# Kernel optimization log

Hardware: AMD Instinct MI355X
Metric: run time of the kernel (lower is better)

## Reference

```python
import jax, jax.numpy as jnp
import numpy as np

COORD_DIM = 4
HIDDEN = 256
N_HIDDEN_LAYERS = 4  # num_layers - 1 hidden->hidden layers after the first
MIN_OMEGA = 10.0
MAX_OMEGA = 100.0
MEDIAN_OMEGA = (MIN_OMEGA + MAX_OMEGA) / 2.0
N = 524288


def _uniform(key, shape, bound):
    return jax.random.uniform(key, shape, jnp.float32, -bound, bound)


def setup_inputs() -> dict:
    key = jax.random.key(0)
    ks = jax.random.split(key, 16)
    coords = jax.random.normal(ks[0], (N, COORD_DIM), jnp.float32)
    # omega predictor: Linear(4, 64) -> ReLU -> Linear(64, 1) -> Sigmoid
    ow1 = _uniform(ks[1], (COORD_DIM, HIDDEN // 4), 1.0 / np.sqrt(COORD_DIM))
    ob1 = _uniform(ks[2], (HIDDEN // 4,), 1.0 / np.sqrt(COORD_DIM))
    ow2 = _uniform(ks[3], (HIDDEN // 4, 1), 1.0 / np.sqrt(HIDDEN // 4))
    ob2 = _uniform(ks[4], (1,), 1.0 / np.sqrt(HIDDEN // 4))
    # SIREN first layer: uniform(-1/in_features, 1/in_features)
    w0 = _uniform(ks[5], (COORD_DIM, HIDDEN), 1.0 / COORD_DIM)
    b0 = _uniform(ks[6], (HIDDEN,), 1.0 / np.sqrt(COORD_DIM))
    # SIREN hidden layers: uniform(-sqrt(6/in)/omega0, ...), stacked [4, 256, 256]
    hb = np.sqrt(6.0 / HIDDEN) / MEDIAN_OMEGA
    wh = _uniform(ks[7], (N_HIDDEN_LAYERS, HIDDEN, HIDDEN), hb)
    bh = _uniform(ks[8], (N_HIDDEN_LAYERS, HIDDEN), 1.0 / np.sqrt(HIDDEN))
    wf = _uniform(ks[9], (HIDDEN, 1), hb)
    bf = _uniform(ks[10], (1,), 1.0 / np.sqrt(HIDDEN))
    return {"coords": coords, "ow1": ow1, "ob1": ob1, "ow2": ow2, "ob2": ob2,
            "w0": w0, "b0": b0, "wh": wh, "bh": bh, "wf": wf, "bf": bf}


def reference(coords, ow1, ob1, ow2, ob2, w0, b0, wh, bh, wf, bf):
    # adaptive omega per coordinate: [N, 1]
    h = jax.nn.relu(coords @ ow1 + ob1)
    omega = MIN_OMEGA + (MAX_OMEGA - MIN_OMEGA) * jax.nn.sigmoid(h @ ow2 + ob2)
    # SIREN stack: x = sin(omega * (x @ W + b))
    x = jnp.sin(omega * (coords @ w0 + b0))
    for i in range(N_HIDDEN_LAYERS):
        x = jnp.sin(omega * (x @ wh[i] + bh[i]))
    return x @ wf + bf  # [N, 1]
```

## Files before the change

### kernel.cpp

```cpp
#include <hip/hip_runtime.h>
#include <hip/hip_bf16.h>

typedef _Float16 f16;
typedef f16 f16x4 __attribute__((ext_vector_type(4)));
typedef f16 f16x8 __attribute__((ext_vector_type(8)));
typedef __fp16 h16x2 __attribute__((ext_vector_type(2)));
typedef __fp16 h16x4 __attribute__((ext_vector_type(4)));
typedef float f32x4 __attribute__((ext_vector_type(4)));
typedef float f32x16 __attribute__((ext_vector_type(16)));

#define MT 128
#define LDST 260
#define INV2PI 0.15915494309189535f

__global__ __launch_bounds__(64)
void prep_wt(const float* __restrict__ wh, f16* __restrict__ wt) {
    const int b = blockIdx.x;
    const int layer = b >> 7, wcblk = (b >> 4) & 7, kblk = b & 15;
    const int lane = threadIdx.x;
    const int l31 = lane & 31, lh = lane >> 5;
    const float* src = wh + layer * 65536 + (kblk * 16 + lh * 8) * 256 + wcblk * 32 + l31;
    f16x8 v;
#pragma unroll
    for (int j = 0; j < 8; j++) v[j] = (f16)src[j * 256];
    *(f16x8*)(wt + b * 512 + lane * 8) = v;
}

__device__ inline f16x8 lds_ld8(const f16* p) {
    f16x4 lo = *(const f16x4*)p;
    f16x4 hi = *(const f16x4*)(p + 4);
    return __builtin_shufflevector(lo, hi, 0, 1, 2, 3, 4, 5, 6, 7);
}

__device__ inline f16x4 pk4(float z0, float z1, float z2, float z3) {
    h16x2 a = __builtin_amdgcn_cvt_pkrtz(z0, z1);
    h16x2 b = __builtin_amdgcn_cvt_pkrtz(z2, z3);
    h16x4 r = __builtin_shufflevector(a, b, 0, 1, 2, 3);
    return __builtin_bit_cast(f16x4, r);
}

__global__ __launch_bounds__(512, 4)
void siren_fused(const float* __restrict__ coords,
                 const float* __restrict__ ow1, const float* __restrict__ ob1,
                 const float* __restrict__ ow2, const float* __restrict__ ob2,
                 const float* __restrict__ w0, const float* __restrict__ b0,
                 const f16* __restrict__ wt,
                 const float* __restrict__ bh,
                 const float* __restrict__ wf,
                 const float* __restrict__ bf,
                 float* __restrict__ out) {
    __shared__ __align__(16) f16 Xs[MT * LDST];
    __shared__ float om_rev[MT];
    __shared__ __align__(16) float crd[MT * 4];
    __shared__ __align__(16) float bh_all[1024];
    __shared__ __align__(16) float wf_s[256];

    const int t = threadIdx.x;
    const long base_pt = (long)blockIdx.x * MT;

    if (t < MT) ((f32x4*)crd)[t] = ((const f32x4*)(coords + base_pt * 4))[t];
    if (t < 256) wf_s[t] = wf[t];
    bh_all[t] = bh[t];
    bh_all[t + 512] = bh[t + 512];
    __syncthreads();

    if (t < MT) {
        const float c0 = crd[t * 4], c1 = crd[t * 4 + 1], c2 = crd[t * 4 + 2], c3 = crd[t * 4 + 3];
        float h[64];
#pragma unroll
        for (int j = 0; j < 64; j++) {
            float z = ob1[j] + c0 * ow1[j] + c1 * ow1[64 + j] + c2 * ow1[128 + j] + c3 * ow1[192 + j];
            h[j] = fmaxf(z, 0.f);
        }
        float z2 = ob2[0];
#pragma unroll
        for (int j = 0; j < 64; j++) z2 += h[j] * ow2[j];
        const float sig = 1.f / (1.f + __expf(-z2));
        om_rev[t] = (10.f + 90.f * sig) * INV2PI;
    }
    __syncthreads();

    {
        const int pt = t >> 2;
        const int q = t & 3;
        const float c0 = crd[pt * 4], c1 = crd[pt * 4 + 1], c2 = crd[pt * 4 + 2], c3 = crd[pt * 4 + 3];
        const float orv = om_rev[pt];
#pragma unroll
        for (int i = 0; i < 4; i++) {
            const int ch = (q + 4 * i) * 16;
#pragma unroll
            for (int c = 0; c < 16; c += 4) {
                f32x4 wv0 = *(const f32x4*)(w0 + 0 * 256 + ch + c);
                f32x4 wv1 = *(const f32x4*)(w0 + 1 * 256 + ch + c);
                f32x4 wv2 = *(const f32x4*)(w0 + 2 * 256 + ch + c);
                f32x4 wv3 = *(const f32x4*)(w0 + 3 * 256 + ch + c);
                f32x4 bv  = *(const f32x4*)(b0 + ch + c);
                float z[4];
#pragma unroll
                for (int j = 0; j < 4; j++) {
                    float zz = bv[j] + c0 * wv0[j] + c1 * wv1[j] + c2 * wv2[j] + c3 * wv3[j];
                    z[j] = orv * __builtin_amdgcn_sinf(orv * zz);
                }
                *(f16x4*)&Xs[pt * LDST + ch + c] = pk4(z[0], z[1], z[2], z[3]);
            }
        }
    }
    __syncthreads();

    const int lane = t & 63;
    const int wave = t >> 6;
    const int l31 = lane & 31;
    const int lh = lane >> 5;
    const int wcg = wave & 3;
    const int pr0 = (wave >> 2) * 64;
    const int wc0 = wcg * 64;

    const f16* bptr = &Xs[(pr0 + l31) * LDST + lh * 8];
    float orv[2];
#pragma unroll
    for (int rt = 0; rt < 2; rt++) orv[rt] = om_rev[pr0 + rt * 32 + l31];

    const f16* afrag0 = wt + ((0 * 8 + wcg * 2) * 16) * 512 + lane * 8;
    f16x8 a0[4], a1[4];
#pragma unroll
    for (int d = 0; d < 4; d++) {
        a0[d] = *(const f16x8*)(afrag0 + d * 512);
        a1[d] = *(const f16x8*)(afrag0 + 8192 + d * 512);
    }

#pragma unroll
    for (int layer = 0; layer < 4; layer++) {
        const f16* afrag = wt + ((layer * 8 + wcg * 2) * 16) * 512 + lane * 8;
        const int next_off = (layer < 3) ? 65536 : -3 * 65536;
        const float* bhl = bh_all + layer * 256;

        f16x8 bv0 = lds_ld8(bptr);
        f16x8 bv1 = lds_ld8(bptr + 32 * LDST);

        f32x16 acc[2][2];
#pragma unroll
        for (int ct = 0; ct < 2; ct++)
#pragma unroll
            for (int g = 0; g < 4; g++) {
                const int wc = wc0 + ct * 32 + g * 8 + lh * 4;
                f32x4 bb = *(const f32x4*)&bhl[wc];
#pragma unroll
                for (int rt = 0; rt < 2; rt++)
#pragma unroll
                    for (int j = 0; j < 4; j++) acc[ct][rt][g * 4 + j] = orv[rt] * bb[j];
            }

#pragma unroll
        for (int kb = 0; kb < 16; kb++) {
            const int s = kb & 3;
            f16x8 av0 = a0[s], av1 = a1[s];
            const int idx = kb + 4;
            const f16* rb = afrag + (idx >= 16 ? next_off : 0) + (idx & 15) * 512;
            a0[s] = *(const f16x8*)rb;
            a1[s] = *(const f16x8*)(rb + 8192);
            f16x8 cb0 = bv0, cb1 = bv1;
            if (kb < 15) {
                bv0 = lds_ld8(bptr + (kb + 1) * 16);
                bv1 = lds_ld8(bptr + 32 * LDST + (kb + 1) * 16);
            }
            acc[0][0] = __builtin_amdgcn_mfma_f32_32x32x16_f16(av0, cb0, acc[0][0], 0, 0, 0);
            acc[0][1] = __builtin_amdgcn_mfma_f32_32x32x16_f16(av0, cb1, acc[0][1], 0, 0, 0);
            acc[1][0] = __builtin_amdgcn_mfma_f32_32x32x16_f16(av1, cb0, acc[1][0], 0, 0, 0);
            acc[1][1] = __builtin_amdgcn_mfma_f32_32x32x16_f16(av1, cb1, acc[1][1], 0, 0, 0);
        }
        __syncthreads();

#pragma unroll
        for (int ct = 0; ct < 2; ct++) {
#pragma unroll
            for (int g = 0; g < 4; g++) {
                const int wc = wc0 + ct * 32 + g * 8 + lh * 4;
#pragma unroll
                for (int rt = 0; rt < 2; rt++) {
                    const int prow = pr0 + rt * 32 + l31;
                    float z[4];
#pragma unroll
                    for (int j = 0; j < 4; j++) {
                        float v = __builtin_amdgcn_sinf(acc[ct][rt][g * 4 + j]);
                        z[j] = (layer < 3) ? orv[rt] * v : v;
                    }
                    *(f16x4*)&Xs[prow * LDST + wc] = pk4(z[0], z[1], z[2], z[3]);
                }
            }
        }
        __syncthreads();
    }

    {
        const int pt = t >> 2;
        const int q = t & 3;
        const f16* xrow = &Xs[pt * LDST];
        float s = 0.f;
#pragma unroll
        for (int i = 0; i < 4; i++) {
            const int ch = (q + 4 * i) * 16;
#pragma unroll
            for (int c = 0; c < 16; c += 4) {
                f16x4 xv = *(const f16x4*)(xrow + ch + c);
                f32x4 wv = *(const f32x4*)&wf_s[ch + c];
                s += (float)xv[0] * wv[0] + (float)xv[1] * wv[1]
                   + (float)xv[2] * wv[2] + (float)xv[3] * wv[3];
            }
        }
        s += __shfl_xor(s, 1, 64);
        s += __shfl_xor(s, 2, 64);
        if (q == 0) out[base_pt + pt] = s + bf[0];
    }
}

extern "C" void kernel_launch(void* const* d_in, const int* in_sizes, int n_in,
                              void* d_out, int out_size, void* d_ws, size_t ws_size,
                              hipStream_t stream) {
    (void)in_sizes; (void)n_in; (void)out_size; (void)ws_size;
    const float* coords = (const float*)d_in[0];
    const float* ow1 = (const float*)d_in[1];
    const float* ob1 = (const float*)d_in[2];
    const float* ow2 = (const float*)d_in[3];
    const float* ob2 = (const float*)d_in[4];
    const float* w0  = (const float*)d_in[5];
    const float* b0  = (const float*)d_in[6];
    const float* wh  = (const float*)d_in[7];
    const float* bh  = (const float*)d_in[8];
    const float* wf  = (const float*)d_in[9];
    const float* bf  = (const float*)d_in[10];
    float* out = (float*)d_out;
    f16* wt = (f16*)d_ws;

    prep_wt<<<512, 64, 0, stream>>>(wh, wt);
    siren_fused<<<524288 / MT, 512, 0, stream>>>(coords, ow1, ob1, ow2, ob2,
                                                 w0, b0, wt, bh, wf, bf, out);
}
```

Baseline: 485.2 us.

## Relax launch bounds, drop B-fragment prefetch, scale omega in packed fp16

Lowers the minimum waves-per-EU hint from 4 to 2, which lets the compiler use more registers per thread. The software prefetch of the next k-step's LDS B fragments is removed, so loads are issued right before their MFMAs. The omega scaling after the sine is moved from fp32 per element to a packed fp16 multiply after conversion. Together these aim to cut register pressure and VALU work, at the cost of less latency hiding and slightly different rounding from multiplying in fp16.

```diff
diff --git a/kernel.cpp b/kernel.cpp
--- a/kernel.cpp
+++ b/kernel.cpp
@@ -39,7 +39,7 @@
     return __builtin_bit_cast(f16x4, r);
 }
 
-__global__ __launch_bounds__(512, 4)
+__global__ __launch_bounds__(512, 2)
 void siren_fused(const float* __restrict__ coords,
                  const float* __restrict__ ow1, const float* __restrict__ ob1,
                  const float* __restrict__ ow2, const float* __restrict__ ob2,
@@ -117,8 +117,12 @@
 
     const f16* bptr = &Xs[(pr0 + l31) * LDST + lh * 8];
     float orv[2];
-#pragma unroll
-    for (int rt = 0; rt < 2; rt++) orv[rt] = om_rev[pr0 + rt * 32 + l31];
+    f16 orv_h[2];
+#pragma unroll
+    for (int rt = 0; rt < 2; rt++) {
+        orv[rt] = om_rev[pr0 + rt * 32 + l31];
+        orv_h[rt] = (f16)orv[rt];
+    }
 
     const f16* afrag0 = wt + ((0 * 8 + wcg * 2) * 16) * 512 + lane * 8;
     f16x8 a0[4], a1[4];
@@ -133,9 +137,6 @@
         const f16* afrag = wt + ((layer * 8 + wcg * 2) * 16) * 512 + lane * 8;
         const int next_off = (layer < 3) ? 65536 : -3 * 65536;
         const float* bhl = bh_all + layer * 256;
-
-        f16x8 bv0 = lds_ld8(bptr);
-        f16x8 bv1 = lds_ld8(bptr + 32 * LDST);
 
         f32x16 acc[2][2];
 #pragma unroll
@@ -158,15 +159,12 @@
             const f16* rb = afrag + (idx >= 16 ? next_off : 0) + (idx & 15) * 512;
             a0[s] = *(const f16x8*)rb;
             a1[s] = *(const f16x8*)(rb + 8192);
-            f16x8 cb0 = bv0, cb1 = bv1;
-            if (kb < 15) {
-                bv0 = lds_ld8(bptr + (kb + 1) * 16);
-                bv1 = lds_ld8(bptr + 32 * LDST + (kb + 1) * 16);
-            }
-            acc[0][0] = __builtin_amdgcn_mfma_f32_32x32x16_f16(av0, cb0, acc[0][0], 0, 0, 0);
-            acc[0][1] = __builtin_amdgcn_mfma_f32_32x32x16_f16(av0, cb1, acc[0][1], 0, 0, 0);
-            acc[1][0] = __builtin_amdgcn_mfma_f32_32x32x16_f16(av1, cb0, acc[1][0], 0, 0, 0);
-            acc[1][1] = __builtin_amdgcn_mfma_f32_32x32x16_f16(av1, cb1, acc[1][1], 0, 0, 0);
+            f16x8 bv0 = lds_ld8(bptr + kb * 16);
+            f16x8 bv1 = lds_ld8(bptr + 32 * LDST + kb * 16);
+            acc[0][0] = __builtin_amdgcn_mfma_f32_32x32x16_f16(av0, bv0, acc[0][0], 0, 0, 0);
+            acc[0][1] = __builtin_amdgcn_mfma_f32_32x32x16_f16(av0, bv1, acc[0][1], 0, 0, 0);
+            acc[1][0] = __builtin_amdgcn_mfma_f32_32x32x16_f16(av1, bv0, acc[1][0], 0, 0, 0);
+            acc[1][1] = __builtin_amdgcn_mfma_f32_32x32x16_f16(av1, bv1, acc[1][1], 0, 0, 0);
         }
         __syncthreads();
 
@@ -180,11 +178,14 @@
                     const int prow = pr0 + rt * 32 + l31;
                     float z[4];
 #pragma unroll
-                    for (int j = 0; j < 4; j++) {
-                        float v = __builtin_amdgcn_sinf(acc[ct][rt][g * 4 + j]);
-                        z[j] = (layer < 3) ? orv[rt] * v : v;
+                    for (int j = 0; j < 4; j++)
+                        z[j] = __builtin_amdgcn_sinf(acc[ct][rt][g * 4 + j]);
+                    f16x4 r = pk4(z[0], z[1], z[2], z[3]);
+                    if (layer < 3) {
+                        const f16 sh = orv_h[rt];
+                        r *= (f16x4){sh, sh, sh, sh};
                     }
-                    *(f16x4*)&Xs[prow * LDST + wc] = pk4(z[0], z[1], z[2], z[3]);
+                    *(f16x4*)&Xs[prow * LDST + wc] = r;
                 }
             }
         }
```

After: 541.4 us. 11.6% more time.
